# Kernel optimization log

Measured on AMD Instinct MI355X. Metric: run time of the kernel, lower is better.

## Reference

```python
import jax, jax.numpy as jnp
import numpy as np

HIGH_T = 0.75
LOW_T = 0.25
EPS = 1e-6


def quantize_four_val(w):
    # {-1, -0.5, 0, 0.5, 1} banding per thresholds (0 band for |w| <= LOW_T)
    return jnp.where(w > HIGH_T, 1.0,
           jnp.where(w > LOW_T, 0.5,
           jnp.where(w < -HIGH_T, -1.0,
           jnp.where(w < -LOW_T, -0.5, 0.0))))


def setup_inputs() -> dict:
    key = jax.random.key(0)
    k1, k2, k3, k4 = jax.random.split(key, 4)
    B, S, D_IN, D_OUT = 4, 2048, 2048, 2048
    x_real = jax.random.normal(k1, (B, S, D_IN), dtype=jnp.float32)
    x_imag = jax.random.normal(k2, (B, S, D_IN), dtype=jnp.float32)
    # unit-normal weights so all four quantization levels are exercised
    weight_re = jax.random.normal(k3, (D_OUT, D_IN), dtype=jnp.float32)
    weight_im = jax.random.normal(k4, (D_OUT, D_IN), dtype=jnp.float32)
    gamma = jnp.ones((2 * D_IN,), dtype=jnp.float32)
    beta = jnp.zeros((2 * D_IN,), dtype=jnp.float32)
    return {"x_real": x_real, "x_imag": x_imag, "weight_re": weight_re,
            "weight_im": weight_im, "gamma": gamma, "beta": beta}


def reference(x_real, x_imag, weight_re, weight_im, gamma, beta):
    d = x_real.shape[-1]
    # LayerNorm over concatenated [real, imag] last dim (2*d)
    x_cat = jnp.concatenate([x_real, x_imag], axis=-1)
    mu = jnp.mean(x_cat, axis=-1, keepdims=True)
    var = jnp.var(x_cat, axis=-1, keepdims=True)
    norm = (x_cat - mu) * jax.lax.rsqrt(var + EPS) * gamma + beta
    nr, ni = norm[..., :d], norm[..., d:]
    # STE: forward uses quantized weights
    qw_re = quantize_four_val(weight_re)
    qw_im = quantize_four_val(weight_im)
    s_re = jnp.mean(jnp.abs(weight_re))
    s_im = jnp.mean(jnp.abs(weight_im))
    y_real = nr @ qw_re.T - ni @ qw_im.T
    y_imag = nr @ qw_im.T + ni @ qw_re.T
    return (y_real * s_re, y_imag * s_im)
```

## Files before the change

kernel.cpp:

```cpp
#include <hip/hip_runtime.h>
#include <hip/hip_bf16.h>

constexpr int D_IN  = 2048;
constexpr int D_OUT = 2048;
constexpr int GM = 4 * 2048;
constexpr int GK = 2 * D_IN;
constexpr int GN = 2 * D_OUT;

typedef __attribute__((ext_vector_type(8))) short bf16x8;
typedef __attribute__((ext_vector_type(4))) float f32x4;

constexpr int QB = 1024;

__device__ inline unsigned short q4bits(float w) {
    if (w >  0.75f) return 0x3F80;
    if (w >  0.25f) return 0x3F00;
    if (w < -0.75f) return 0xBF80;
    if (w < -0.25f) return 0xBF00;
    return 0;
}

__device__ inline unsigned short bf16b(float x) {
    __hip_bfloat16 h = __float2bfloat16(x);
    unsigned short u;
    __builtin_memcpy(&u, &h, 2);
    return u;
}

__global__ __launch_bounds__(256) void quant_kernel(
        const float* __restrict__ wre, const float* __restrict__ wim,
        unsigned short* __restrict__ wq, float* __restrict__ partial) {
    float a = 0.f, b = 0.f;
    int tid = blockIdx.x * 256 + threadIdx.x;
    const float4* wre4 = (const float4*)wre;
    const float4* wim4 = (const float4*)wim;
    for (int c = 0; c < 4; c++) {
        int f4i = tid + c * (QB * 256);
        int idx = f4i * 4;
        int o = idx >> 11;
        int k = idx & (D_IN - 1);
        float4 r = wre4[f4i];
        float4 im = wim4[f4i];
        a += fabsf(r.x) + fabsf(r.y) + fabsf(r.z) + fabsf(r.w);
        b += fabsf(im.x) + fabsf(im.y) + fabsf(im.z) + fabsf(im.w);
        ushort4 qre, qim, nim;
        qre.x = q4bits(r.x);  qre.y = q4bits(r.y);  qre.z = q4bits(r.z);  qre.w = q4bits(r.w);
        qim.x = q4bits(im.x); qim.y = q4bits(im.y); qim.z = q4bits(im.z); qim.w = q4bits(im.w);
        nim.x = qim.x ^ 0x8000; nim.y = qim.y ^ 0x8000;
        nim.z = qim.z ^ 0x8000; nim.w = qim.w ^ 0x8000;
        *(ushort4*)(wq + (size_t)o * GK + k)                  = qre;
        *(ushort4*)(wq + (size_t)o * GK + D_IN + k)           = nim;
        *(ushort4*)(wq + (size_t)(D_OUT + o) * GK + k)        = qim;
        *(ushort4*)(wq + (size_t)(D_OUT + o) * GK + D_IN + k) = qre;
    }
    for (int off = 32; off; off >>= 1) {
        a += __shfl_down(a, off, 64);
        b += __shfl_down(b, off, 64);
    }
    __shared__ float sa[4], sb[4];
    int lane = threadIdx.x & 63, wv = threadIdx.x >> 6;
    if (lane == 0) { sa[wv] = a; sb[wv] = b; }
    __syncthreads();
    if (threadIdx.x == 0) {
        partial[blockIdx.x]      = sa[0] + sa[1] + sa[2] + sa[3];
        partial[QB + blockIdx.x] = sb[0] + sb[1] + sb[2] + sb[3];
    }
}

__global__ __launch_bounds__(256) void reduce_kernel(
        const float* __restrict__ partial, float* __restrict__ sums) {
    int t = threadIdx.x;
    float a = 0.f, b = 0.f;
    for (int i = t; i < QB; i += 256) { a += partial[i]; b += partial[QB + i]; }
    for (int off = 32; off; off >>= 1) {
        a += __shfl_down(a, off, 64);
        b += __shfl_down(b, off, 64);
    }
    __shared__ float sa[4], sb[4];
    int lane = t & 63, wv = t >> 6;
    if (lane == 0) { sa[wv] = a; sb[wv] = b; }
    __syncthreads();
    if (t == 0) {
        sums[0] = sa[0] + sa[1] + sa[2] + sa[3];
        sums[1] = sb[0] + sb[1] + sb[2] + sb[3];
    }
}

__global__ __launch_bounds__(256) void ln_kernel(
        const float* __restrict__ xr, const float* __restrict__ xi,
        const float* __restrict__ gamma, const float* __restrict__ beta,
        unsigned short* __restrict__ A) {
    int m = blockIdx.x;
    int t = threadIdx.x;
    const float4* r4 = (const float4*)(xr + (size_t)m * D_IN);
    const float4* i4 = (const float4*)(xi + (size_t)m * D_IN);
    float4 vr[2], vi[2];
    float s = 0.f, ss = 0.f;
    for (int c = 0; c < 2; c++) {
        float4 v = r4[t + c * 256];
        vr[c] = v;
        s  += v.x + v.y + v.z + v.w;
        ss += v.x * v.x + v.y * v.y + v.z * v.z + v.w * v.w;
        v = i4[t + c * 256];
        vi[c] = v;
        s  += v.x + v.y + v.z + v.w;
        ss += v.x * v.x + v.y * v.y + v.z * v.z + v.w * v.w;
    }
    for (int off = 32; off; off >>= 1) {
        s  += __shfl_down(s, off, 64);
        ss += __shfl_down(ss, off, 64);
    }
    __shared__ float red[8];
    __shared__ float smu, srs;
    int lane = t & 63, wv = t >> 6;
    if (lane == 0) { red[wv] = s; red[4 + wv] = ss; }
    __syncthreads();
    if (t == 0) {
        float S  = red[0] + red[1] + red[2] + red[3];
        float SS = red[4] + red[5] + red[6] + red[7];
        float mu  = S * (1.0f / 4096.0f);
        float var = SS * (1.0f / 4096.0f) - mu * mu;
        smu = mu;
        srs = rsqrtf(var + 1e-6f);
    }
    __syncthreads();
    float mu = smu, rs = srs;
    const float4* g4 = (const float4*)gamma;
    const float4* b4 = (const float4*)beta;
    ushort4* Arow = (ushort4*)(A + (size_t)m * GK);
    for (int c = 0; c < 2; c++) {
        int k4 = t + c * 256;
        float4 g = g4[k4], b = b4[k4];
        float4 v = vr[c];
        ushort4 o;
        o.x = bf16b((v.x - mu) * rs * g.x + b.x);
        o.y = bf16b((v.y - mu) * rs * g.y + b.y);
        o.z = bf16b((v.z - mu) * rs * g.z + b.z);
        o.w = bf16b((v.w - mu) * rs * g.w + b.w);
        Arow[k4] = o;
        g = g4[512 + k4]; b = b4[512 + k4];
        v = vi[c];
        o.x = bf16b((v.x - mu) * rs * g.x + b.x);
        o.y = bf16b((v.y - mu) * rs * g.y + b.y);
        o.z = bf16b((v.z - mu) * rs * g.z + b.z);
        o.w = bf16b((v.w - mu) * rs * g.w + b.w);
        Arow[512 + k4] = o;
    }
}

__global__ __launch_bounds__(256, 2) void gemm_kernel(
        const unsigned short* __restrict__ A,
        const unsigned short* __restrict__ Wq,
        const float* __restrict__ sums,
        float* __restrict__ out) {
    constexpr int BM = 128, BN = 128, BK = 64;
    __shared__ unsigned short lsA[BM * BK];
    __shared__ unsigned short lsB[BN * BK];
    int n0 = blockIdx.x * BN;
    int m0 = blockIdx.y * BM;
    int t = threadIdx.x, lane = t & 63, wave = t >> 6;
    int wm = (wave >> 1) * 64;
    int wn = (wave & 1) * 64;
    int quad = lane >> 4, r = lane & 15;
    int srow = lane >> 3;
    int scol = ((lane & 7) ^ srow) * 8;

    int csw0 = ((quad ^ (r & 7)) * 8);

    f32x4 acc[4][4] = {};

    for (int k0 = 0; k0 < GK; k0 += BK) {
        for (int i = 0; i < 4; i++) {
            int row = i * 32 + wave * 8;
            const unsigned short* gp = A + (size_t)(m0 + row + srow) * GK + k0 + scol;
            unsigned short* lp = lsA + row * BK;
            __builtin_amdgcn_global_load_lds(
                (const __attribute__((address_space(1))) void*)(const void*)gp,
                (__attribute__((address_space(3))) void*)(void*)lp, 16, 0, 0);
        }
        for (int i = 0; i < 4; i++) {
            int row = i * 32 + wave * 8;
            const unsigned short* gp = Wq + (size_t)(n0 + row + srow) * GK + k0 + scol;
            unsigned short* lp = lsB + row * BK;
            __builtin_amdgcn_global_load_lds(
                (const __attribute__((address_space(1))) void*)(const void*)gp,
                (__attribute__((address_space(3))) void*)(void*)lp, 16, 0, 0);
        }
        __syncthreads();
        for (int ks = 0; ks < 2; ks++) {
            bf16x8 af[4], bfr[4];
            const short* pa = (const short*)lsA;
            const short* pb = (const short*)lsB;
            int coff = csw0 ^ (ks * 32);
            for (int i = 0; i < 4; i++)
                af[i] = *(const bf16x8*)(pa + (wm + i * 16 + r) * BK + coff);
            for (int j = 0; j < 4; j++)
                bfr[j] = *(const bf16x8*)(pb + (wn + j * 16 + r) * BK + coff);
            for (int i = 0; i < 4; i++)
                for (int j = 0; j < 4; j++)
                    acc[i][j] = __builtin_amdgcn_mfma_f32_16x16x32_bf16(
                        af[i], bfr[j], acc[i][j], 0, 0, 0);
        }
        __syncthreads();
    }

    float s_re = sums[0] * (1.0f / (2048.0f * 2048.0f));
    float s_im = sums[1] * (1.0f / (2048.0f * 2048.0f));
    float scale;
    float* obase;
    int ncol0;
    if (n0 < D_OUT) { scale = s_re; obase = out;                        ncol0 = n0; }
    else            { scale = s_im; obase = out + (size_t)GM * D_OUT;   ncol0 = n0 - D_OUT; }

    for (int i = 0; i < 4; i++)
        for (int j = 0; j < 4; j++) {
            int mrow = m0 + wm + i * 16 + quad * 4;
            int ncol = ncol0 + wn + j * 16 + r;
            for (int reg = 0; reg < 4; reg++)
                obase[(size_t)(mrow + reg) * D_OUT + ncol] = acc[i][j][reg] * scale;
        }
}

extern "C" void kernel_launch(void* const* d_in, const int* in_sizes, int n_in,
                              void* d_out, int out_size, void* d_ws, size_t ws_size,
                              hipStream_t stream) {
    const float* xr    = (const float*)d_in[0];
    const float* xi    = (const float*)d_in[1];
    const float* wre   = (const float*)d_in[2];
    const float* wim   = (const float*)d_in[3];
    const float* gamma = (const float*)d_in[4];
    const float* beta  = (const float*)d_in[5];
    float* out = (float*)d_out;

    unsigned short* A  = (unsigned short*)d_ws;
    unsigned short* Wq = (unsigned short*)((char*)d_ws + (size_t)GM * GK * 2);
    float* partial = (float*)((char*)d_ws + (size_t)GM * GK * 2 + (size_t)GN * GK * 2);
    float* sums = partial + 2 * QB;

    quant_kernel<<<QB, 256, 0, stream>>>(wre, wim, Wq, partial);
    reduce_kernel<<<1, 256, 0, stream>>>(partial, sums);
    ln_kernel<<<GM, 256, 0, stream>>>(xr, xi, gamma, beta, A);
    gemm_kernel<<<dim3(GN / 128, GM / 128), 256, 0, stream>>>(A, Wq, sums, out);
}
```

Measured before the change: 489.6 us.

## Double-buffer 256x256 GEMM tile with 8 waves, staged prefetch, and atomic scale reduction

The GEMM is rebuilt around a 256x256x64 tile run by 512 threads. LDS is double-buffered, and the next k-tile is prefetched in four chunks placed between MFMA quadrants, with explicit waitcnt, barriers and setprio. A grid swizzle is added to improve L2 reuse. The separate reduce kernel is replaced by atomicAdd into zeroed sums. The larger tile and double buffer use 128KB of LDS and many more accumulator registers, which likely limits occupancy to one block per CU despite the launch bound of 2.

After: 584.6 us. 19.4% more time.

```diff
diff --git a/kernel.cpp b/kernel.cpp
--- a/kernel.cpp
+++ b/kernel.cpp
@@ -29,7 +29,7 @@
 
 __global__ __launch_bounds__(256) void quant_kernel(
         const float* __restrict__ wre, const float* __restrict__ wim,
-        unsigned short* __restrict__ wq, float* __restrict__ partial) {
+        unsigned short* __restrict__ wq, float* __restrict__ sums) {
     float a = 0.f, b = 0.f;
     int tid = blockIdx.x * 256 + threadIdx.x;
     const float4* wre4 = (const float4*)wre;
@@ -62,27 +62,8 @@
     if (lane == 0) { sa[wv] = a; sb[wv] = b; }
     __syncthreads();
     if (threadIdx.x == 0) {
-        partial[blockIdx.x]      = sa[0] + sa[1] + sa[2] + sa[3];
-        partial[QB + blockIdx.x] = sb[0] + sb[1] + sb[2] + sb[3];
-    }
-}
-
-__global__ __launch_bounds__(256) void reduce_kernel(
-        const float* __restrict__ partial, float* __restrict__ sums) {
-    int t = threadIdx.x;
-    float a = 0.f, b = 0.f;
-    for (int i = t; i < QB; i += 256) { a += partial[i]; b += partial[QB + i]; }
-    for (int off = 32; off; off >>= 1) {
-        a += __shfl_down(a, off, 64);
-        b += __shfl_down(b, off, 64);
-    }
-    __shared__ float sa[4], sb[4];
-    int lane = t & 63, wv = t >> 6;
-    if (lane == 0) { sa[wv] = a; sb[wv] = b; }
-    __syncthreads();
-    if (t == 0) {
-        sums[0] = sa[0] + sa[1] + sa[2] + sa[3];
-        sums[1] = sb[0] + sb[1] + sb[2] + sb[3];
+        atomicAdd(&sums[0], sa[0] + sa[1] + sa[2] + sa[3]);
+        atomicAdd(&sums[1], sb[0] + sb[1] + sb[2] + sb[3]);
     }
 }
 
@@ -148,76 +129,144 @@
     }
 }
 
-__global__ __launch_bounds__(256, 2) void gemm_kernel(
+__global__ __launch_bounds__(512, 2) void gemm_kernel(
         const unsigned short* __restrict__ A,
         const unsigned short* __restrict__ Wq,
         const float* __restrict__ sums,
         float* __restrict__ out) {
-    constexpr int BM = 128, BN = 128, BK = 64;
-    __shared__ unsigned short lsA[BM * BK];
-    __shared__ unsigned short lsB[BN * BK];
-    int n0 = blockIdx.x * BN;
-    int m0 = blockIdx.y * BM;
-    int t = threadIdx.x, lane = t & 63, wave = t >> 6;
-    int wm = (wave >> 1) * 64;
-    int wn = (wave & 1) * 64;
+    constexpr int BM = 256, BN = 256, BK = 64;
+    constexpr int NT = GK / BK;
+    __shared__ unsigned short shA[2][BM * BK];
+    __shared__ unsigned short shB[2][BN * BK];
+
+    int lin = blockIdx.y * gridDim.x + blockIdx.x;
+    int swz = (lin & 7) * 64 + (lin >> 3);
+    int m0 = (swz >> 4) * BM;
+    int n0 = (swz & 15) * BN;
+
+    int t = threadIdx.x;
+    int lane = t & 63, wid = t >> 6;
+    int wr = wid >> 2, wc = wid & 3;
     int quad = lane >> 4, r = lane & 15;
     int srow = lane >> 3;
     int scol = ((lane & 7) ^ srow) * 8;
-
-    int csw0 = ((quad ^ (r & 7)) * 8);
-
-    f32x4 acc[4][4] = {};
-
-    for (int k0 = 0; k0 < GK; k0 += BK) {
-        for (int i = 0; i < 4; i++) {
-            int row = i * 32 + wave * 8;
-            const unsigned short* gp = A + (size_t)(m0 + row + srow) * GK + k0 + scol;
-            unsigned short* lp = lsA + row * BK;
-            __builtin_amdgcn_global_load_lds(
-                (const __attribute__((address_space(1))) void*)(const void*)gp,
-                (__attribute__((address_space(3))) void*)(void*)lp, 16, 0, 0);
-        }
-        for (int i = 0; i < 4; i++) {
-            int row = i * 32 + wave * 8;
-            const unsigned short* gp = Wq + (size_t)(n0 + row + srow) * GK + k0 + scol;
-            unsigned short* lp = lsB + row * BK;
-            __builtin_amdgcn_global_load_lds(
-                (const __attribute__((address_space(1))) void*)(const void*)gp,
-                (__attribute__((address_space(3))) void*)(void*)lp, 16, 0, 0);
-        }
-        __syncthreads();
-        for (int ks = 0; ks < 2; ks++) {
-            bf16x8 af[4], bfr[4];
-            const short* pa = (const short*)lsA;
-            const short* pb = (const short*)lsB;
-            int coff = csw0 ^ (ks * 32);
-            for (int i = 0; i < 4; i++)
-                af[i] = *(const bf16x8*)(pa + (wm + i * 16 + r) * BK + coff);
-            for (int j = 0; j < 4; j++)
-                bfr[j] = *(const bf16x8*)(pb + (wn + j * 16 + r) * BK + coff);
-            for (int i = 0; i < 4; i++)
-                for (int j = 0; j < 4; j++)
-                    acc[i][j] = __builtin_amdgcn_mfma_f32_16x16x32_bf16(
-                        af[i], bfr[j], acc[i][j], 0, 0, 0);
-        }
-        __syncthreads();
-    }
+    int csw0 = (quad ^ (r & 7)) * 8;
+
+    int aRow0 = (wr * 128 + r) * BK;
+    int bRow0 = (wc * 64 + r) * BK;
+
+    f32x4 acc[8][4] = {};
+    bf16x8 a[4][2], b[2][2];
+
+#define STAGE(mm, bb, kk, ss) do {                                             \
+        int dstRow = wid * 32 + (ss) * 8;                                      \
+        const unsigned short* gsrc =                                           \
+            ((mm) ? Wq + (size_t)(n0 + dstRow + srow) * GK                     \
+                  : A  + (size_t)(m0 + dstRow + srow) * GK)                    \
+            + (kk) * BK + scol;                                                \
+        unsigned short* lp = ((mm) ? shB[bb] : shA[bb]) + dstRow * BK;         \
+        __builtin_amdgcn_global_load_lds(                                      \
+            (const __attribute__((address_space(1))) void*)(const void*)gsrc,  \
+            (__attribute__((address_space(3))) void*)(void*)lp, 16, 0, 0);     \
+    } while (0)
+
+#define READ_A(mh) do {                                                        \
+        const short* pa_ = (const short*)shA[cur];                             \
+        _Pragma("unroll") for (int im = 0; im < 4; ++im)                       \
+        _Pragma("unroll") for (int ks = 0; ks < 2; ++ks)                       \
+            a[im][ks] = *(const bf16x8*)(pa_ + aRow0                           \
+                + ((mh) * 4 + im) * (16 * BK) + (csw0 ^ (ks * 32)));           \
+    } while (0)
+
+#define READ_B(nh) do {                                                        \
+        const short* pb_ = (const short*)shB[cur];                             \
+        _Pragma("unroll") for (int jn = 0; jn < 2; ++jn)                       \
+        _Pragma("unroll") for (int ks = 0; ks < 2; ++ks)                       \
+            b[jn][ks] = *(const bf16x8*)(pb_ + bRow0                           \
+                + ((nh) * 2 + jn) * (16 * BK) + (csw0 ^ (ks * 32)));           \
+    } while (0)
+
+#define MFMA_Q(mh, nh) do {                                                    \
+        __builtin_amdgcn_s_setprio(1);                                         \
+        _Pragma("unroll") for (int im = 0; im < 4; ++im)                       \
+        _Pragma("unroll") for (int jn = 0; jn < 2; ++jn)                       \
+        _Pragma("unroll") for (int ks = 0; ks < 2; ++ks)                       \
+            acc[(mh) * 4 + im][(nh) * 2 + jn] =                                \
+                __builtin_amdgcn_mfma_f32_16x16x32_bf16(                       \
+                    a[im][ks], b[jn][ks],                                      \
+                    acc[(mh) * 4 + im][(nh) * 2 + jn], 0, 0, 0);               \
+        __builtin_amdgcn_s_setprio(0);                                         \
+    } while (0)
+
+    #pragma unroll
+    for (int ss = 0; ss < 4; ++ss) STAGE(0, 0, 0, ss);
+    #pragma unroll
+    for (int ss = 0; ss < 4; ++ss) STAGE(1, 0, 0, ss);
+
+    #pragma unroll 2
+    for (int kt = 0; kt < NT; ++kt) {
+        int cur = kt & 1, nxt = cur ^ 1;
+        bool more = (kt < NT - 1);
+
+        __builtin_amdgcn_sched_barrier(0);
+        if (more) { STAGE(0, nxt, kt + 1, 0); STAGE(0, nxt, kt + 1, 1); }
+        if (more) asm volatile("s_waitcnt vmcnt(2)" ::: "memory");
+        else      asm volatile("s_waitcnt vmcnt(0)" ::: "memory");
+        __builtin_amdgcn_s_barrier();
+        __builtin_amdgcn_sched_barrier(0);
+        READ_A(0); READ_B(0);
+        asm volatile("s_waitcnt lgkmcnt(0)" ::: "memory");
+        __builtin_amdgcn_sched_barrier(0);
+        MFMA_Q(0, 0);
+        __builtin_amdgcn_s_barrier();
+
+        READ_B(1);
+        if (more) { STAGE(0, nxt, kt + 1, 2); STAGE(0, nxt, kt + 1, 3); }
+        __builtin_amdgcn_s_barrier();
+        asm volatile("s_waitcnt lgkmcnt(0)" ::: "memory");
+        __builtin_amdgcn_sched_barrier(0);
+        MFMA_Q(0, 1);
+        __builtin_amdgcn_s_barrier();
+
+        READ_A(1);
+        if (more) { STAGE(1, nxt, kt + 1, 0); STAGE(1, nxt, kt + 1, 1); }
+        __builtin_amdgcn_s_barrier();
+        asm volatile("s_waitcnt lgkmcnt(0)" ::: "memory");
+        __builtin_amdgcn_sched_barrier(0);
+        MFMA_Q(1, 1);
+        __builtin_amdgcn_s_barrier();
+
+        READ_B(0);
+        if (more) { STAGE(1, nxt, kt + 1, 2); STAGE(1, nxt, kt + 1, 3); }
+        __builtin_amdgcn_s_barrier();
+        asm volatile("s_waitcnt lgkmcnt(0)" ::: "memory");
+        __builtin_amdgcn_sched_barrier(0);
+        MFMA_Q(1, 0);
+        __builtin_amdgcn_s_barrier();
+    }
+
+#undef STAGE
+#undef READ_A
+#undef READ_B
+#undef MFMA_Q
 
     float s_re = sums[0] * (1.0f / (2048.0f * 2048.0f));
     float s_im = sums[1] * (1.0f / (2048.0f * 2048.0f));
     float scale;
     float* obase;
     int ncol0;
-    if (n0 < D_OUT) { scale = s_re; obase = out;                        ncol0 = n0; }
-    else            { scale = s_im; obase = out + (size_t)GM * D_OUT;   ncol0 = n0 - D_OUT; }
-
-    for (int i = 0; i < 4; i++)
-        for (int j = 0; j < 4; j++) {
-            int mrow = m0 + wm + i * 16 + quad * 4;
-            int ncol = ncol0 + wn + j * 16 + r;
-            for (int reg = 0; reg < 4; reg++)
-                obase[(size_t)(mrow + reg) * D_OUT + ncol] = acc[i][j][reg] * scale;
+    if (n0 < D_OUT) { scale = s_re; obase = out;                      ncol0 = n0; }
+    else            { scale = s_im; obase = out + (size_t)GM * D_OUT; ncol0 = n0 - D_OUT; }
+
+    #pragma unroll
+    for (int f = 0; f < 8; ++f)
+        #pragma unroll
+        for (int g = 0; g < 4; ++g) {
+            int mrow = m0 + wr * 128 + f * 16 + quad * 4;
+            int ncol = ncol0 + wc * 64 + g * 16 + r;
+            #pragma unroll
+            for (int reg = 0; reg < 4; ++reg)
+                obase[(size_t)(mrow + reg) * D_OUT + ncol] = acc[f][g][reg] * scale;
         }
 }
 
@@ -234,11 +283,10 @@
 
     unsigned short* A  = (unsigned short*)d_ws;
     unsigned short* Wq = (unsigned short*)((char*)d_ws + (size_t)GM * GK * 2);
-    float* partial = (float*)((char*)d_ws + (size_t)GM * GK * 2 + (size_t)GN * GK * 2);
-    float* sums = partial + 2 * QB;
-
-    quant_kernel<<<QB, 256, 0, stream>>>(wre, wim, Wq, partial);
-    reduce_kernel<<<1, 256, 0, stream>>>(partial, sums);
+    float* sums = (float*)((char*)d_ws + (size_t)GM * GK * 2 + (size_t)GN * GK * 2);
+
+    (void)hipMemsetAsync(sums, 0, 2 * sizeof(float), stream);
+    quant_kernel<<<QB, 256, 0, stream>>>(wre, wim, Wq, sums);
     ln_kernel<<<GM, 256, 0, stream>>>(xr, xi, gamma, beta, A);
-    gemm_kernel<<<dim3(GN / 128, GM / 128), 256, 0, stream>>>(A, Wq, sums, out);
-}
+    gemm_kernel<<<dim3(GN / 256, GM / 256), 512, 0, stream>>>(A, Wq, sums, out);
+}
```

## Double-buffer GEMM LDS tiles and replace reduce kernel with atomics

Applied to the files above, without the earlier changes.

The GEMM now keeps two LDS buffers for the A and B tiles and issues the global-to-LDS loads for the next K tile before computing on the current one. It uses explicit vmcnt waits and raw barriers so the loads overlap with the MFMA work. The separate reduce kernel is removed: each quant block atomically adds its partial abs-sums into a buffer cleared by hipMemsetAsync. This saves a launch but makes the float summation order nondeterministic, and doubling LDS to 64KB per block may limit how many blocks fit on a CU.

Result: slower. 528.1 us (+7.9%).

```diff
diff --git a/kernel.cpp b/kernel.cpp
--- a/kernel.cpp
+++ b/kernel.cpp
@@ -29,7 +29,7 @@
 
 __global__ __launch_bounds__(256) void quant_kernel(
         const float* __restrict__ wre, const float* __restrict__ wim,
-        unsigned short* __restrict__ wq, float* __restrict__ partial) {
+        unsigned short* __restrict__ wq, float* __restrict__ sums) {
     float a = 0.f, b = 0.f;
     int tid = blockIdx.x * 256 + threadIdx.x;
     const float4* wre4 = (const float4*)wre;
@@ -62,27 +62,8 @@
     if (lane == 0) { sa[wv] = a; sb[wv] = b; }
     __syncthreads();
     if (threadIdx.x == 0) {
-        partial[blockIdx.x]      = sa[0] + sa[1] + sa[2] + sa[3];
-        partial[QB + blockIdx.x] = sb[0] + sb[1] + sb[2] + sb[3];
-    }
-}
-
-__global__ __launch_bounds__(256) void reduce_kernel(
-        const float* __restrict__ partial, float* __restrict__ sums) {
-    int t = threadIdx.x;
-    float a = 0.f, b = 0.f;
-    for (int i = t; i < QB; i += 256) { a += partial[i]; b += partial[QB + i]; }
-    for (int off = 32; off; off >>= 1) {
-        a += __shfl_down(a, off, 64);
-        b += __shfl_down(b, off, 64);
-    }
-    __shared__ float sa[4], sb[4];
-    int lane = t & 63, wv = t >> 6;
-    if (lane == 0) { sa[wv] = a; sb[wv] = b; }
-    __syncthreads();
-    if (t == 0) {
-        sums[0] = sa[0] + sa[1] + sa[2] + sa[3];
-        sums[1] = sb[0] + sb[1] + sb[2] + sb[3];
+        atomicAdd(&sums[0], sa[0] + sa[1] + sa[2] + sa[3]);
+        atomicAdd(&sums[1], sb[0] + sb[1] + sb[2] + sb[3]);
     }
 }
 
@@ -154,8 +135,9 @@
         const float* __restrict__ sums,
         float* __restrict__ out) {
     constexpr int BM = 128, BN = 128, BK = 64;
-    __shared__ unsigned short lsA[BM * BK];
-    __shared__ unsigned short lsB[BN * BK];
+    constexpr int NT = GK / BK;
+    __shared__ unsigned short lsA[2][BM * BK];
+    __shared__ unsigned short lsB[2][BN * BK];
     int n0 = blockIdx.x * BN;
     int m0 = blockIdx.y * BM;
     int t = threadIdx.x, lane = t & 63, wave = t >> 6;
@@ -164,33 +146,51 @@
     int quad = lane >> 4, r = lane & 15;
     int srow = lane >> 3;
     int scol = ((lane & 7) ^ srow) * 8;
-
     int csw0 = ((quad ^ (r & 7)) * 8);
 
     f32x4 acc[4][4] = {};
 
-    for (int k0 = 0; k0 < GK; k0 += BK) {
-        for (int i = 0; i < 4; i++) {
-            int row = i * 32 + wave * 8;
-            const unsigned short* gp = A + (size_t)(m0 + row + srow) * GK + k0 + scol;
-            unsigned short* lp = lsA + row * BK;
-            __builtin_amdgcn_global_load_lds(
-                (const __attribute__((address_space(1))) void*)(const void*)gp,
-                (__attribute__((address_space(3))) void*)(void*)lp, 16, 0, 0);
+#define STAGE_TILE(bb, kk) do {                                                \
+        for (int i_ = 0; i_ < 4; i_++) {                                       \
+            int row_ = i_ * 32 + wave * 8;                                     \
+            const unsigned short* gp_ =                                        \
+                A + (size_t)(m0 + row_ + srow) * GK + (kk) * BK + scol;        \
+            unsigned short* lp_ = lsA[bb] + row_ * BK;                         \
+            __builtin_amdgcn_global_load_lds(                                  \
+                (const __attribute__((address_space(1))) void*)(const void*)gp_,\
+                (__attribute__((address_space(3))) void*)(void*)lp_, 16, 0, 0);\
+        }                                                                      \
+        for (int i_ = 0; i_ < 4; i_++) {                                       \
+            int row_ = i_ * 32 + wave * 8;                                     \
+            const unsigned short* gp_ =                                        \
+                Wq + (size_t)(n0 + row_ + srow) * GK + (kk) * BK + scol;       \
+            unsigned short* lp_ = lsB[bb] + row_ * BK;                         \
+            __builtin_amdgcn_global_load_lds(                                  \
+                (const __attribute__((address_space(1))) void*)(const void*)gp_,\
+                (__attribute__((address_space(3))) void*)(void*)lp_, 16, 0, 0);\
+        }                                                                      \
+    } while (0)
+
+    STAGE_TILE(0, 0);
+
+    #pragma unroll 2
+    for (int kt = 0; kt < NT; ++kt) {
+        int cur = kt & 1, nxt = cur ^ 1;
+
+        __builtin_amdgcn_sched_barrier(0);
+        if (kt + 1 < NT) {
+            STAGE_TILE(nxt, kt + 1);
+            asm volatile("s_waitcnt vmcnt(8)" ::: "memory");
+        } else {
+            asm volatile("s_waitcnt vmcnt(0)" ::: "memory");
         }
-        for (int i = 0; i < 4; i++) {
-            int row = i * 32 + wave * 8;
-            const unsigned short* gp = Wq + (size_t)(n0 + row + srow) * GK + k0 + scol;
-            unsigned short* lp = lsB + row * BK;
-            __builtin_amdgcn_global_load_lds(
-                (const __attribute__((address_space(1))) void*)(const void*)gp,
-                (__attribute__((address_space(3))) void*)(void*)lp, 16, 0, 0);
-        }
-        __syncthreads();
+        __builtin_amdgcn_s_barrier();
+        __builtin_amdgcn_sched_barrier(0);
+
+        const short* pa = (const short*)lsA[cur];
+        const short* pb = (const short*)lsB[cur];
         for (int ks = 0; ks < 2; ks++) {
             bf16x8 af[4], bfr[4];
-            const short* pa = (const short*)lsA;
-            const short* pb = (const short*)lsB;
             int coff = csw0 ^ (ks * 32);
             for (int i = 0; i < 4; i++)
                 af[i] = *(const bf16x8*)(pa + (wm + i * 16 + r) * BK + coff);
@@ -201,8 +201,11 @@
                     acc[i][j] = __builtin_amdgcn_mfma_f32_16x16x32_bf16(
                         af[i], bfr[j], acc[i][j], 0, 0, 0);
         }
-        __syncthreads();
-    }
+        asm volatile("s_waitcnt lgkmcnt(0)" ::: "memory");
+        __builtin_amdgcn_sched_barrier(0);
+        __builtin_amdgcn_s_barrier();
+    }
+#undef STAGE_TILE
 
     float s_re = sums[0] * (1.0f / (2048.0f * 2048.0f));
     float s_im = sums[1] * (1.0f / (2048.0f * 2048.0f));
@@ -234,11 +237,10 @@
 
     unsigned short* A  = (unsigned short*)d_ws;
     unsigned short* Wq = (unsigned short*)((char*)d_ws + (size_t)GM * GK * 2);
-    float* partial = (float*)((char*)d_ws + (size_t)GM * GK * 2 + (size_t)GN * GK * 2);
-    float* sums = partial + 2 * QB;
-
-    quant_kernel<<<QB, 256, 0, stream>>>(wre, wim, Wq, partial);
-    reduce_kernel<<<1, 256, 0, stream>>>(partial, sums);
+    float* sums = (float*)((char*)d_ws + (size_t)GM * GK * 2 + (size_t)GN * GK * 2);
+
+    (void)hipMemsetAsync(sums, 0, 2 * sizeof(float), stream);
+    quant_kernel<<<QB, 256, 0, stream>>>(wre, wim, Wq, sums);
     ln_kernel<<<GM, 256, 0, stream>>>(xr, xi, gamma, beta, A);
     gemm_kernel<<<dim3(GN / 128, GM / 128), 256, 0, stream>>>(A, Wq, sums, out);
 }
```
